# Optimization experiments

Hardware: AMD Instinct MI355X
Metric: run time of the kernel (lower is better)

Reference implementation:

```python
import jax, jax.numpy as jnp
import numpy as np

NEG_SLOPE = 0.2  # PyG GATConv leaky_relu slope


def _add_self_loops(edge_index, num_nodes):
    loops = jnp.arange(num_nodes, dtype=edge_index.dtype)
    src = jnp.concatenate([edge_index[0], loops])
    dst = jnp.concatenate([edge_index[1], loops])
    return src, dst


def _gat_conv(x, src, dst, W, a_src, a_dst, b, num_nodes):
    # W: [in, H*F]; a_src, a_dst: [H, F]; b: [H*F]
    H, F = a_src.shape
    h = (x @ W).reshape(num_nodes, H, F)                # [N,H,F]
    alpha_src = jnp.einsum('nhf,hf->nh', h, a_src)      # [N,H]
    alpha_dst = jnp.einsum('nhf,hf->nh', h, a_dst)      # [N,H]
    logits = alpha_src[src] + alpha_dst[dst]            # [E,H]
    logits = jax.nn.leaky_relu(logits, NEG_SLOPE)
    # segment softmax over incoming edges of each dst node
    seg_max = jax.ops.segment_max(logits, dst, num_segments=num_nodes)  # [N,H]
    e = jnp.exp(logits - seg_max[dst])                  # [E,H]
    denom = jax.ops.segment_sum(e, dst, num_segments=num_nodes)         # [N,H]
    alpha = e / denom[dst]                              # [E,H] (self-loops guarantee denom>0)
    msg = h[src] * alpha[:, :, None]                    # [E,H,F]
    out = jax.ops.segment_sum(msg, dst, num_segments=num_nodes)         # [N,H,F]
    return out.reshape(num_nodes, H * F) + b            # concat=True


def _gcn_conv(x, src, dst, W, b, num_nodes):
    h = x @ W                                           # [N,out]
    ones = jnp.ones(dst.shape[0], dtype=h.dtype)
    deg = jax.ops.segment_sum(ones, dst, num_segments=num_nodes)        # [N]
    dinv = jnp.where(deg > 0, jax.lax.rsqrt(deg), 0.0)
    norm = dinv[src] * dinv[dst]                        # [E]
    out = jax.ops.segment_sum(h[src] * norm[:, None], dst, num_segments=num_nodes)
    return out + b


def setup_inputs() -> dict:
    key = jax.random.key(0)
    ks = jax.random.split(key, 10)
    N, E = 50000, 800000
    in_dim, hid, H1, ncls = 128, 32, 8, 16
    s = 0.05
    d = {}
    d['x'] = jax.random.normal(ks[0], (N, in_dim), jnp.float32)
    d['edge_index'] = jax.random.randint(ks[1], (2, E), 0, N)
    # GATConv 1: in=128 -> hid=32, heads=8
    d['W1'] = jax.random.normal(ks[2], (in_dim, H1 * hid), jnp.float32) * s
    d['a_src1'] = jax.random.normal(ks[3], (H1, hid), jnp.float32) * s
    d['a_dst1'] = jax.random.normal(ks[4], (H1, hid), jnp.float32) * s
    d['b1'] = jnp.zeros((H1 * hid,), jnp.float32)
    # GATConv 2: in=256 -> hid//2=16, heads=1
    d['W2'] = jax.random.normal(ks[5], (H1 * hid, hid // 2), jnp.float32) * s
    d['a_src2'] = jax.random.normal(ks[6], (1, hid // 2), jnp.float32) * s
    d['a_dst2'] = jax.random.normal(ks[7], (1, hid // 2), jnp.float32) * s
    d['b2'] = jnp.zeros((hid // 2,), jnp.float32)
    # GCNConv: 16 -> 16 classes
    d['W3'] = jax.random.normal(ks[8], (hid // 2, ncls), jnp.float32) * s
    d['b3'] = jnp.zeros((ncls,), jnp.float32)
    return d


def reference(x, edge_index, W1, a_src1, a_dst1, b1, W2, a_src2, a_dst2, b2, W3, b3):
    N = x.shape[0]
    src, dst = _add_self_loops(edge_index, N)
    # dropout layers are identity in eval mode
    h = _gat_conv(x, src, dst, W1, a_src1, a_dst1, b1, N)
    h = jax.nn.elu(h)
    h = _gat_conv(h, src, dst, W2, a_src2, a_dst2, b2, N)
    h = jax.nn.elu(h)
    out = _gcn_conv(h, src, dst, W3, b3, N)
    return out
```

## Files before the change

### kernel.cpp

```cpp
#include <hip/hip_runtime.h>
#include <hip/hip_bf16.h>
#include <math.h>

#define NEG_SLOPE 0.2f

typedef float f32x4 __attribute__((ext_vector_type(4)));
typedef short bf16x8 __attribute__((ext_vector_type(8)));
typedef unsigned int u32x2 __attribute__((ext_vector_type(2)));

static __device__ __forceinline__ float lrelu(float x) { return x > 0.f ? x : NEG_SLOPE * x; }
static __device__ __forceinline__ float elu1(float x)  { return x > 0.f ? x : (expf(x) - 1.f); }

static __device__ __forceinline__ unsigned short f2bf(float x) {
    __hip_bfloat16 h = __float2bfloat16(x);
    return *reinterpret_cast<unsigned short*>(&h);
}
static __device__ __forceinline__ unsigned int pack2bf(float a, float b) {
    return (unsigned int)f2bf(a) | ((unsigned int)f2bf(b) << 16);
}
static __device__ __forceinline__ float bflo(unsigned int u) { return __uint_as_float(u << 16); }
static __device__ __forceinline__ float bfhi(unsigned int u) { return __uint_as_float(u & 0xFFFF0000u); }

__global__ void count_kernel(const int* __restrict__ ei, int* __restrict__ counts, int E, int E2) {
    int i = blockIdx.x * blockDim.x + threadIdx.x;
    if (i >= E2) return;
    int dst = (i < E) ? ei[E + i] : (i - E);
    atomicAdd(&counts[dst], 1);
}

__global__ __launch_bounds__(256) void scanA_kernel(const int* __restrict__ counts, int* __restrict__ blocksum, int N) {
    __shared__ int red[256];
    int t = threadIdx.x;
    int i = blockIdx.x * 256 + t;
    int v = (i < N) ? counts[i] : 0;
    red[t] = v; __syncthreads();
    for (int off = 128; off >= 1; off >>= 1) {
        if (t < off) red[t] += red[t + off];
        __syncthreads();
    }
    if (t == 0) blocksum[blockIdx.x] = red[0];
}

__global__ __launch_bounds__(256) void scanB_kernel(int* __restrict__ bs, int NB) {
    __shared__ int sm[256];
    int t = threadIdx.x;
    int carry = 0;
    for (int b0 = 0; b0 < NB; b0 += 256) {
        int v = (b0 + t < NB) ? bs[b0 + t] : 0;
        sm[t] = v; __syncthreads();
        for (int off = 1; off < 256; off <<= 1) {
            int u = (t >= off) ? sm[t - off] : 0;
            __syncthreads();
            sm[t] += u;
            __syncthreads();
        }
        if (b0 + t < NB) bs[b0 + t] = carry + sm[t] - v;
        int tot = sm[255];
        __syncthreads();
        carry += tot;
    }
}

__global__ __launch_bounds__(256) void scanC_kernel(const int* __restrict__ counts, const int* __restrict__ blocksum,
                                                    int* __restrict__ row_start, int* __restrict__ fillc,
                                                    float* __restrict__ dinv, int N) {
    __shared__ int sm[256];
    int t = threadIdx.x;
    int i = blockIdx.x * 256 + t;
    int v = (i < N) ? counts[i] : 0;
    sm[t] = v; __syncthreads();
    for (int off = 1; off < 256; off <<= 1) {
        int u = (t >= off) ? sm[t - off] : 0;
        __syncthreads();
        sm[t] += u;
        __syncthreads();
    }
    if (i < N) {
        int rsv = blocksum[blockIdx.x] + sm[t] - v;
        row_start[i] = rsv;
        fillc[i] = rsv;
        dinv[i] = rsqrtf((float)v);
    }
    if (i == N - 1) row_start[N] = blocksum[blockIdx.x] + sm[t];
}

__global__ void fill_kernel(const int* __restrict__ ei, int* __restrict__ fillc,
                            int* __restrict__ srcs, int E, int E2) {
    int i = blockIdx.x * blockDim.x + threadIdx.x;
    if (i >= E2) return;
    int src, dst;
    if (i < E) { src = ei[i]; dst = ei[E + i]; }
    else       { src = i - E; dst = i - E; }
    int pos = atomicAdd(&fillc[dst], 1);
    srcs[pos] = src;
}

__global__ __launch_bounds__(256) void prepW_kernel(const float* __restrict__ W1, unsigned short* __restrict__ Wb) {
    int idx = blockIdx.x * 256 + threadIdx.x;
    int j = idx & 7;
    int lane = (idx >> 3) & 63;
    int t = (idx >> 9) & 15;
    int kk = idx >> 13;
    int k = kk * 32 + (lane >> 4) * 8 + j;
    int n = t * 16 + (lane & 15);
    Wb[idx] = f2bf(W1[k * 256 + n]);
}

__global__ __launch_bounds__(256) void gemm1_kernel(const float* __restrict__ x, const unsigned short* __restrict__ Wb,
                                                    const float* __restrict__ a_src, const float* __restrict__ a_dst,
                                                    unsigned short* __restrict__ h1b, float* __restrict__ as1,
                                                    float* __restrict__ ad1, int M) {
    int w = threadIdx.x >> 6, lane = threadIdx.x & 63;
    int quad = lane >> 4, c = lane & 15;
    int rowA = blockIdx.x * 64 + w * 16 + c;
    int rowAc = rowA < M ? rowA : M - 1;
    f32x4 acc[16];
    #pragma unroll
    for (int t = 0; t < 16; t++) acc[t] = (f32x4){0.f, 0.f, 0.f, 0.f};
    #pragma unroll
    for (int kk = 0; kk < 4; kk++) {
        const float* ap = &x[(size_t)rowAc * 128 + kk * 32 + quad * 8];
        float4 a0 = *(const float4*)ap;
        float4 a1 = *(const float4*)(ap + 4);
        union { bf16x8 v; unsigned int u[4]; } af;
        af.u[0] = pack2bf(a0.x, a0.y); af.u[1] = pack2bf(a0.z, a0.w);
        af.u[2] = pack2bf(a1.x, a1.y); af.u[3] = pack2bf(a1.z, a1.w);
        const bf16x8* bp = (const bf16x8*)&Wb[(size_t)(kk * 16) * 512 + lane * 8];
        #pragma unroll
        for (int t = 0; t < 16; t++) {
            bf16x8 bf = bp[t * 64];
            acc[t] = __builtin_amdgcn_mfma_f32_16x16x32_bf16(af.v, bf, acc[t], 0, 0, 0);
        }
    }
    int growb = blockIdx.x * 64 + w * 16 + quad * 4;
    #pragma unroll
    for (int r = 0; r < 4; r++) {
        int grow = growb + r;
        if (grow < M) {
            #pragma unroll
            for (int t = 0; t < 16; t++)
                h1b[(size_t)grow * 256 + t * 16 + c] = f2bf(acc[t][r]);
        }
    }
    float asA[8], asB[8], adA[8], adB[8];
    #pragma unroll
    for (int h = 0; h < 8; h++) {
        asA[h] = a_src[h * 32 + c];      asB[h] = a_src[h * 32 + 16 + c];
        adA[h] = a_dst[h * 32 + c];      adB[h] = a_dst[h * 32 + 16 + c];
    }
    #pragma unroll
    for (int r = 0; r < 4; r++) {
        int grow = growb + r;
        #pragma unroll
        for (int h = 0; h < 8; h++) {
            float ps = acc[2 * h][r] * asA[h] + acc[2 * h + 1][r] * asB[h];
            float pd = acc[2 * h][r] * adA[h] + acc[2 * h + 1][r] * adB[h];
            ps += __shfl_xor(ps, 1); ps += __shfl_xor(ps, 2); ps += __shfl_xor(ps, 4); ps += __shfl_xor(ps, 8);
            pd += __shfl_xor(pd, 1); pd += __shfl_xor(pd, 2); pd += __shfl_xor(pd, 4); pd += __shfl_xor(pd, 8);
            if (c == 0 && grow < M) { as1[grow * 8 + h] = ps; ad1[grow * 8 + h] = pd; }
        }
    }
}

__global__ __launch_bounds__(256) void agg1_kernel(const unsigned short* __restrict__ h1b, const float* __restrict__ asrc,
                                                   const float* __restrict__ adst, const int* __restrict__ row_start,
                                                   const int* __restrict__ srcs, const float* __restrict__ b1,
                                                   unsigned short* __restrict__ h1pb, int N) {
    int node = blockIdx.x * 4 + (threadIdx.x >> 6);
    if (node >= N) return;
    int lane = threadIdx.x & 63;
    int h = lane >> 3, e8 = lane & 7;
    float adn = adst[node * 8 + h];
    int rs = row_start[node], re = row_start[node + 1];
    float4 acc = make_float4(0.f, 0.f, 0.f, 0.f);
    float den = 0.f;
    int o4 = lane * 4;
    for (int base = rs; base < re; base += 64) {
        int cnt = re - base; if (cnt > 64) cnt = 64;
        int sv = __builtin_nontemporal_load(&srcs[base + (lane < cnt ? lane : 0)]);
        int g = 0;
        for (; g + 16 <= cnt; g += 16) {
            int ssA = __shfl(sv, g + e8);
            int ssB = __shfl(sv, g + 8 + e8);
            float wA = __expf(lrelu(asrc[ssA * 8 + h] + adn));
            float wB = __expf(lrelu(asrc[ssB * 8 + h] + adn));
            uint2 v[16];
            #pragma unroll
            for (int q = 0; q < 16; q++) {
                int s = __shfl(sv, g + q);
                v[q] = *(const uint2*)&h1b[(size_t)s * 256 + o4];
            }
            #pragma unroll
            for (int q = 0; q < 8; q++) {
                float w = __shfl(wA, (h << 3) | q);
                acc.x += w * bflo(v[q].x); acc.y += w * bfhi(v[q].x);
                acc.z += w * bflo(v[q].y); acc.w += w * bfhi(v[q].y);
                den += w;
            }
            #pragma unroll
            for (int q = 8; q < 16; q++) {
                float w = __shfl(wB, (h << 3) | (q - 8));
                acc.x += w * bflo(v[q].x); acc.y += w * bfhi(v[q].x);
                acc.z += w * bflo(v[q].y); acc.w += w * bfhi(v[q].y);
                den += w;
            }
        }
        if (g + 8 <= cnt) {
            int ss = __shfl(sv, g + e8);
            float wp = __expf(lrelu(asrc[ss * 8 + h] + adn));
            uint2 v[8];
            #pragma unroll
            for (int q = 0; q < 8; q++) {
                int s = __shfl(sv, g + q);
                v[q] = *(const uint2*)&h1b[(size_t)s * 256 + o4];
            }
            #pragma unroll
            for (int q = 0; q < 8; q++) {
                float w = __shfl(wp, (h << 3) | q);
                acc.x += w * bflo(v[q].x); acc.y += w * bfhi(v[q].x);
                acc.z += w * bflo(v[q].y); acc.w += w * bfhi(v[q].y);
                den += w;
            }
            g += 8;
        }
        if (g < cnt) {
            int ep = g + e8;
            int epc = ep < cnt - 1 ? ep : cnt - 1;
            int ss = __shfl(sv, epc);
            float wp = (ep < cnt) ? __expf(lrelu(asrc[ss * 8 + h] + adn)) : 0.f;
            #pragma unroll
            for (int q = 0; q < 8; q++) {
                if (g + q < cnt) {
                    int s = __shfl(sv, g + q);
                    float w = __shfl(wp, (h << 3) | q);
                    uint2 vv = *(const uint2*)&h1b[(size_t)s * 256 + o4];
                    acc.x += w * bflo(vv.x); acc.y += w * bfhi(vv.x);
                    acc.z += w * bflo(vv.y); acc.w += w * bfhi(vv.y);
                    den += w;
                }
            }
        }
    }
    float inv = 1.f / den;
    u32x2 r;
    r.x = pack2bf(elu1(acc.x * inv + b1[o4 + 0]), elu1(acc.y * inv + b1[o4 + 1]));
    r.y = pack2bf(elu1(acc.z * inv + b1[o4 + 2]), elu1(acc.w * inv + b1[o4 + 3]));
    __builtin_nontemporal_store(r, (u32x2*)&h1pb[(size_t)node * 256 + o4]);
}

__global__ __launch_bounds__(256) void gemm2_kernel(const unsigned short* __restrict__ X, const float* __restrict__ W2,
                                                    const float* __restrict__ a_src2, const float* __restrict__ a_dst2,
                                                    float* __restrict__ h2, float* __restrict__ asrc2,
                                                    float* __restrict__ adst2, int N) {
    int lane = threadIdx.x & 63;
    int c = lane & 15, kq = lane >> 4;
    int wid = blockIdx.x * (blockDim.x >> 6) + (threadIdx.x >> 6);
    int nwaves = gridDim.x * (blockDim.x >> 6);
    float w2r[64];
    #pragma unroll
    for (int i = 0; i < 64; i++) w2r[i] = W2[(kq * 64 + i) * 16 + c];
    float as_c = a_src2[c], ad_c = a_dst2[c];
    for (int n = wid; n < N; n += nwaves) {
        const unsigned short* xp = &X[(size_t)n * 256 + kq * 64];
        float acc = 0.f;
        #pragma unroll
        for (int i8 = 0; i8 < 8; i8++) {
            uint4 xv = *(const uint4*)&xp[i8 * 8];
            int b = i8 * 8;
            acc += bflo(xv.x) * w2r[b+0] + bfhi(xv.x) * w2r[b+1]
                 + bflo(xv.y) * w2r[b+2] + bfhi(xv.y) * w2r[b+3]
                 + bflo(xv.z) * w2r[b+4] + bfhi(xv.z) * w2r[b+5]
                 + bflo(xv.w) * w2r[b+6] + bfhi(xv.w) * w2r[b+7];
        }
        acc += __shfl_xor(acc, 16);
        acc += __shfl_xor(acc, 32);
        float s1 = acc * as_c, s2 = acc * ad_c;
        #pragma unroll
        for (int off = 1; off < 16; off <<= 1) { s1 += __shfl_xor(s1, off); s2 += __shfl_xor(s2, off); }
        if (kq == 0) h2[n * 16 + c] = acc;
        if (lane == 0) { asrc2[n] = s1; adst2[n] = s2; }
    }
}

__global__ __launch_bounds__(256) void agg2_kernel(const float* __restrict__ h2, const float* __restrict__ asrc2,
                                                   const float* __restrict__ adst2, const int* __restrict__ row_start,
                                                   const int* __restrict__ srcs, const float* __restrict__ b2,
                                                   const float* __restrict__ W3, float* __restrict__ h4, int N) {
    int node = blockIdx.x * 4 + (threadIdx.x >> 6);
    if (node >= N) return;
    int lane = threadIdx.x & 63;
    int q = lane >> 4, c = lane & 15;
    float adn = adst2[node];
    int rs = row_start[node], re = row_start[node + 1];
    float acc = 0.f, den = 0.f;
    for (int base = rs; base < re; base += 64) {
        int cnt = re - base; if (cnt > 64) cnt = 64;
        int sv = 0; float wv = 0.f;
        if (lane < cnt) { sv = __builtin_nontemporal_load(&srcs[base + lane]); wv = __expf(lrelu(asrc2[sv] + adn)); }
        int nit = (cnt + 3) >> 2;
        int it = 0;
        for (; it + 4 <= nit; it += 4) {
            int s0 = __shfl(sv, it * 4 + q),       s1 = __shfl(sv, (it + 1) * 4 + q);
            int s2 = __shfl(sv, (it + 2) * 4 + q), s3 = __shfl(sv, (it + 3) * 4 + q);
            float w0 = __shfl(wv, it * 4 + q),       w1 = __shfl(wv, (it + 1) * 4 + q);
            float w2 = __shfl(wv, (it + 2) * 4 + q), w3 = __shfl(wv, (it + 3) * 4 + q);
            float v0 = h2[s0 * 16 + c], v1 = h2[s1 * 16 + c];
            float v2 = h2[s2 * 16 + c], v3 = h2[s3 * 16 + c];
            acc += w0 * v0 + w1 * v1 + w2 * v2 + w3 * v3;
            den += (w0 + w1) + (w2 + w3);
        }
        for (; it < nit; it++) {
            int j = it * 4 + q;
            int s = __shfl(sv, j);
            float w = __shfl(wv, j);
            acc += w * h2[s * 16 + c]; den += w;
        }
    }
    acc += __shfl_xor(acc, 16); acc += __shfl_xor(acc, 32);
    den += __shfl_xor(den, 16); den += __shfl_xor(den, 32);
    float h3v = elu1(acc / den + b2[c]);
    float h4v = 0.f;
    #pragma unroll
    for (int cs = 0; cs < 16; cs++) {
        float hv = __shfl(h3v, cs);
        h4v += hv * W3[cs * 16 + c];
    }
    if (q == 0) h4[node * 16 + c] = h4v;
}

__global__ __launch_bounds__(256) void agg3_kernel(const float* __restrict__ h4, const float* __restrict__ dinv,
                                                   const int* __restrict__ row_start, const int* __restrict__ srcs,
                                                   const float* __restrict__ b3, float* __restrict__ out, int N) {
    int node = blockIdx.x * 4 + (threadIdx.x >> 6);
    if (node >= N) return;
    int lane = threadIdx.x & 63;
    int q = lane >> 4, c = lane & 15;
    int rs = row_start[node], re = row_start[node + 1];
    float acc = 0.f;
    for (int base = rs; base < re; base += 64) {
        int cnt = re - base; if (cnt > 64) cnt = 64;
        int sv = 0; float wv = 0.f;
        if (lane < cnt) { sv = __builtin_nontemporal_load(&srcs[base + lane]); wv = dinv[sv]; }
        int nit = (cnt + 3) >> 2;
        int it = 0;
        for (; it + 4 <= nit; it += 4) {
            int s0 = __shfl(sv, it * 4 + q),       s1 = __shfl(sv, (it + 1) * 4 + q);
            int s2 = __shfl(sv, (it + 2) * 4 + q), s3 = __shfl(sv, (it + 3) * 4 + q);
            float w0 = __shfl(wv, it * 4 + q),       w1 = __shfl(wv, (it + 1) * 4 + q);
            float w2 = __shfl(wv, (it + 2) * 4 + q), w3 = __shfl(wv, (it + 3) * 4 + q);
            float v0 = h4[s0 * 16 + c], v1 = h4[s1 * 16 + c];
            float v2 = h4[s2 * 16 + c], v3 = h4[s3 * 16 + c];
            acc += w0 * v0 + w1 * v1 + w2 * v2 + w3 * v3;
        }
        for (; it < nit; it++) {
            int j = it * 4 + q;
            int s = __shfl(sv, j);
            float w = __shfl(wv, j);
            acc += w * h4[s * 16 + c];
        }
    }
    acc += __shfl_xor(acc, 16); acc += __shfl_xor(acc, 32);
    if (q == 0) out[node * 16 + c] = acc * dinv[node] + b3[c];
}

extern "C" void kernel_launch(void* const* d_in, const int* in_sizes, int n_in,
                              void* d_out, int out_size, void* d_ws, size_t ws_size,
                              hipStream_t stream) {
    const float* x      = (const float*)d_in[0];
    const int*   ei     = (const int*)d_in[1];
    const float* W1     = (const float*)d_in[2];
    const float* a_src1 = (const float*)d_in[3];
    const float* a_dst1 = (const float*)d_in[4];
    const float* b1     = (const float*)d_in[5];
    const float* W2     = (const float*)d_in[6];
    const float* a_src2 = (const float*)d_in[7];
    const float* a_dst2 = (const float*)d_in[8];
    const float* b2     = (const float*)d_in[9];
    const float* W3     = (const float*)d_in[10];
    const float* b3     = (const float*)d_in[11];
    float* out = (float*)d_out;

    const int N  = in_sizes[0] / 128;
    const int E  = in_sizes[1] / 2;
    const int E2 = E + N;
    const int NB = (N + 255) / 256;

    char* p = (char*)d_ws;
    auto alloc = [&](size_t bytes) -> void* {
        void* r = (void*)p;
        p += (bytes + 255) & ~(size_t)255;
        return r;
    };
    int*   counts = (int*)alloc((size_t)N * 4);
    int*   rowst  = (int*)alloc((size_t)(N + 1) * 4);
    int*   fillc  = (int*)alloc((size_t)N * 4);
    int*   srcs   = (int*)alloc((size_t)E2 * 4);
    int*   bsum   = (int*)alloc((size_t)NB * 4);
    unsigned short* Wb   = (unsigned short*)alloc((size_t)32768 * 2);
    unsigned short* h1b  = (unsigned short*)alloc((size_t)N * 256 * 2);
    unsigned short* h1pb = (unsigned short*)alloc((size_t)N * 256 * 2);
    float* as1    = (float*)alloc((size_t)N * 8 * 4);
    float* ad1    = (float*)alloc((size_t)N * 8 * 4);
    float* h2     = (float*)alloc((size_t)N * 16 * 4);
    float* as2    = (float*)alloc((size_t)N * 4);
    float* ad2    = (float*)alloc((size_t)N * 4);
    float* h4     = (float*)alloc((size_t)N * 16 * 4);
    float* dinv   = (float*)alloc((size_t)N * 4);

    (void)hipMemsetAsync(counts, 0, (size_t)N * 4, stream);

    count_kernel<<<(E2 + 255) / 256, 256, 0, stream>>>(ei, counts, E, E2);
    scanA_kernel<<<NB, 256, 0, stream>>>(counts, bsum, N);
    scanB_kernel<<<1, 256, 0, stream>>>(bsum, NB);
    scanC_kernel<<<NB, 256, 0, stream>>>(counts, bsum, rowst, fillc, dinv, N);
    fill_kernel<<<(E2 + 255) / 256, 256, 0, stream>>>(ei, fillc, srcs, E, E2);

    prepW_kernel<<<128, 256, 0, stream>>>(W1, Wb);
    gemm1_kernel<<<(N + 63) / 64, 256, 0, stream>>>(x, Wb, a_src1, a_dst1, h1b, as1, ad1, N);
    agg1_kernel<<<(N + 3) / 4, 256, 0, stream>>>(h1b, as1, ad1, rowst, srcs, b1, h1pb, N);

    gemm2_kernel<<<1024, 256, 0, stream>>>(h1pb, W2, a_src2, a_dst2, h2, as2, ad2, N);
    agg2_kernel<<<(N + 3) / 4, 256, 0, stream>>>(h2, as2, ad2, rowst, srcs, b2, W3, h4, N);

    agg3_kernel<<<(N + 3) / 4, 256, 0, stream>>>(h4, dinv, rowst, srcs, b3, out, N);
}
```

Baseline: 365.9 us.

## Fuse CSR build and weight prep into one cooperative kernel with grid syncs

Replaces the memset plus six small kernels (count, three scan stages, fill, W1 bf16 prep) with a single cooperative kernel of 1024 blocks that uses grid-wide syncs between phases. This targets per-launch overhead and the idle gaps between tiny dependent kernels. In exchange it adds grid barrier costs, and the atomic count and fill phases now run with grid-stride loops over fewer threads. The cooperative launch requires all 1024 blocks to be co-resident on the device.

New measurement: 858.7 us. 2.35x slower.

```diff
diff --git a/kernel.cpp b/kernel.cpp
--- a/kernel.cpp
+++ b/kernel.cpp
@@ -1,6 +1,9 @@
 #include <hip/hip_runtime.h>
+#include <hip/hip_cooperative_groups.h>
 #include <hip/hip_bf16.h>
 #include <math.h>
+
+namespace cg = cooperative_groups;
 
 #define NEG_SLOPE 0.2f
 
@@ -21,89 +24,91 @@
 static __device__ __forceinline__ float bflo(unsigned int u) { return __uint_as_float(u << 16); }
 static __device__ __forceinline__ float bfhi(unsigned int u) { return __uint_as_float(u & 0xFFFF0000u); }
 
-__global__ void count_kernel(const int* __restrict__ ei, int* __restrict__ counts, int E, int E2) {
-    int i = blockIdx.x * blockDim.x + threadIdx.x;
-    if (i >= E2) return;
-    int dst = (i < E) ? ei[E + i] : (i - E);
-    atomicAdd(&counts[dst], 1);
-}
-
-__global__ __launch_bounds__(256) void scanA_kernel(const int* __restrict__ counts, int* __restrict__ blocksum, int N) {
-    __shared__ int red[256];
-    int t = threadIdx.x;
-    int i = blockIdx.x * 256 + t;
-    int v = (i < N) ? counts[i] : 0;
-    red[t] = v; __syncthreads();
-    for (int off = 128; off >= 1; off >>= 1) {
-        if (t < off) red[t] += red[t + off];
+__global__ __launch_bounds__(256) void csr_kernel(const int* __restrict__ ei, const float* __restrict__ W1,
+                                                  int* __restrict__ counts, int* __restrict__ bsum,
+                                                  int* __restrict__ row_start, int* __restrict__ fillc,
+                                                  float* __restrict__ dinv, int* __restrict__ srcs,
+                                                  unsigned short* __restrict__ Wb,
+                                                  int N, int E, int E2, int NB) {
+    cg::grid_group grid = cg::this_grid();
+    const int tid = blockIdx.x * 256 + threadIdx.x;
+    const int nth = gridDim.x * 256;
+    __shared__ int sm[256];
+
+    for (int i = tid; i < N; i += nth) counts[i] = 0;
+    for (int idx = tid; idx < 32768; idx += nth) {
+        int j = idx & 7, lane = (idx >> 3) & 63, t = (idx >> 9) & 15, kk = idx >> 13;
+        int k = kk * 32 + (lane >> 4) * 8 + j;
+        int n = t * 16 + (lane & 15);
+        Wb[idx] = f2bf(W1[k * 256 + n]);
+    }
+    grid.sync();
+
+    for (int i = tid; i < E2; i += nth) {
+        int dst = (i < E) ? ei[E + i] : (i - E);
+        atomicAdd(&counts[dst], 1);
+    }
+    grid.sync();
+
+    for (int tile = blockIdx.x; tile < NB; tile += gridDim.x) {
+        int i = tile * 256 + threadIdx.x;
+        int v = (i < N) ? counts[i] : 0;
+        sm[threadIdx.x] = v; __syncthreads();
+        for (int off = 128; off >= 1; off >>= 1) {
+            if (threadIdx.x < off) sm[threadIdx.x] += sm[threadIdx.x + off];
+            __syncthreads();
+        }
+        if (threadIdx.x == 0) bsum[tile] = sm[0];
         __syncthreads();
     }
-    if (t == 0) blocksum[blockIdx.x] = red[0];
-}
-
-__global__ __launch_bounds__(256) void scanB_kernel(int* __restrict__ bs, int NB) {
-    __shared__ int sm[256];
-    int t = threadIdx.x;
-    int carry = 0;
-    for (int b0 = 0; b0 < NB; b0 += 256) {
-        int v = (b0 + t < NB) ? bs[b0 + t] : 0;
+    grid.sync();
+
+    if (blockIdx.x == 0) {
+        int t = threadIdx.x;
+        int carry = 0;
+        for (int b0 = 0; b0 < NB; b0 += 256) {
+            int v = (b0 + t < NB) ? bsum[b0 + t] : 0;
+            sm[t] = v; __syncthreads();
+            for (int off = 1; off < 256; off <<= 1) {
+                int u = (t >= off) ? sm[t - off] : 0;
+                __syncthreads();
+                sm[t] += u; __syncthreads();
+            }
+            if (b0 + t < NB) bsum[b0 + t] = carry + sm[t] - v;
+            int tot = sm[255]; __syncthreads();
+            carry += tot;
+        }
+    }
+    grid.sync();
+
+    for (int tile = blockIdx.x; tile < NB; tile += gridDim.x) {
+        int t = threadIdx.x;
+        int i = tile * 256 + t;
+        int v = (i < N) ? counts[i] : 0;
         sm[t] = v; __syncthreads();
         for (int off = 1; off < 256; off <<= 1) {
             int u = (t >= off) ? sm[t - off] : 0;
             __syncthreads();
-            sm[t] += u;
-            __syncthreads();
-        }
-        if (b0 + t < NB) bs[b0 + t] = carry + sm[t] - v;
-        int tot = sm[255];
+            sm[t] += u; __syncthreads();
+        }
+        if (i < N) {
+            int rsv = bsum[tile] + sm[t] - v;
+            row_start[i] = rsv;
+            fillc[i] = rsv;
+            dinv[i] = rsqrtf((float)v);
+        }
+        if (i == N - 1) row_start[N] = bsum[tile] + sm[t];
         __syncthreads();
-        carry += tot;
-    }
-}
-
-__global__ __launch_bounds__(256) void scanC_kernel(const int* __restrict__ counts, const int* __restrict__ blocksum,
-                                                    int* __restrict__ row_start, int* __restrict__ fillc,
-                                                    float* __restrict__ dinv, int N) {
-    __shared__ int sm[256];
-    int t = threadIdx.x;
-    int i = blockIdx.x * 256 + t;
-    int v = (i < N) ? counts[i] : 0;
-    sm[t] = v; __syncthreads();
-    for (int off = 1; off < 256; off <<= 1) {
-        int u = (t >= off) ? sm[t - off] : 0;
-        __syncthreads();
-        sm[t] += u;
-        __syncthreads();
-    }
-    if (i < N) {
-        int rsv = blocksum[blockIdx.x] + sm[t] - v;
-        row_start[i] = rsv;
-        fillc[i] = rsv;
-        dinv[i] = rsqrtf((float)v);
-    }
-    if (i == N - 1) row_start[N] = blocksum[blockIdx.x] + sm[t];
-}
-
-__global__ void fill_kernel(const int* __restrict__ ei, int* __restrict__ fillc,
-                            int* __restrict__ srcs, int E, int E2) {
-    int i = blockIdx.x * blockDim.x + threadIdx.x;
-    if (i >= E2) return;
-    int src, dst;
-    if (i < E) { src = ei[i]; dst = ei[E + i]; }
-    else       { src = i - E; dst = i - E; }
-    int pos = atomicAdd(&fillc[dst], 1);
-    srcs[pos] = src;
-}
-
-__global__ __launch_bounds__(256) void prepW_kernel(const float* __restrict__ W1, unsigned short* __restrict__ Wb) {
-    int idx = blockIdx.x * 256 + threadIdx.x;
-    int j = idx & 7;
-    int lane = (idx >> 3) & 63;
-    int t = (idx >> 9) & 15;
-    int kk = idx >> 13;
-    int k = kk * 32 + (lane >> 4) * 8 + j;
-    int n = t * 16 + (lane & 15);
-    Wb[idx] = f2bf(W1[k * 256 + n]);
+    }
+    grid.sync();
+
+    for (int i = tid; i < E2; i += nth) {
+        int src, dst;
+        if (i < E) { src = ei[i]; dst = ei[E + i]; }
+        else       { src = i - E; dst = i - E; }
+        int pos = atomicAdd(&fillc[dst], 1);
+        srcs[pos] = src;
+    }
 }
 
 __global__ __launch_bounds__(256) void gemm1_kernel(const float* __restrict__ x, const unsigned short* __restrict__ Wb,
@@ -407,15 +412,14 @@
     float* h4     = (float*)alloc((size_t)N * 16 * 4);
     float* dinv   = (float*)alloc((size_t)N * 4);
 
-    (void)hipMemsetAsync(counts, 0, (size_t)N * 4, stream);
-
-    count_kernel<<<(E2 + 255) / 256, 256, 0, stream>>>(ei, counts, E, E2);
-    scanA_kernel<<<NB, 256, 0, stream>>>(counts, bsum, N);
-    scanB_kernel<<<1, 256, 0, stream>>>(bsum, NB);
-    scanC_kernel<<<NB, 256, 0, stream>>>(counts, bsum, rowst, fillc, dinv, N);
-    fill_kernel<<<(E2 + 255) / 256, 256, 0, stream>>>(ei, fillc, srcs, E, E2);
-
-    prepW_kernel<<<128, 256, 0, stream>>>(W1, Wb);
+    {
+        int n_ = N, e_ = E, e2_ = E2, nb_ = NB;
+        void* args[] = { (void*)&ei, (void*)&W1, (void*)&counts, (void*)&bsum, (void*)&rowst,
+                         (void*)&fillc, (void*)&dinv, (void*)&srcs, (void*)&Wb,
+                         (void*)&n_, (void*)&e_, (void*)&e2_, (void*)&nb_ };
+        (void)hipLaunchCooperativeKernel((void*)csr_kernel, dim3(1024), dim3(256), args, 0, stream);
+    }
+
     gemm1_kernel<<<(N + 63) / 64, 256, 0, stream>>>(x, Wb, a_src1, a_dst1, h1b, as1, ad1, N);
     agg1_kernel<<<(N + 3) / 4, 256, 0, stream>>>(h1b, as1, ad1, rowst, srcs, b1, h1pb, N);
 
```
